# Performance work log

Measured on AMD Instinct MI355X. Metric: run time of the kernel, lower is better.

Reference implementation:

```python
import jax, jax.numpy as jnp
import numpy as np

NEG_SLOPE = 0.2


def gat_conv(x, src, dst, W, att_src, att_dst, bias, heads, out_ch, concat):
    # PyG GATConv (add_self_loops handled by caller). x: [N, in], W: [heads*out, in]
    N = x.shape[0]
    xw = (x @ W.T).reshape(N, heads, out_ch)                  # [N, H, C]
    a_src = jnp.sum(xw * att_src, axis=-1)                    # [N, H]
    a_dst = jnp.sum(xw * att_dst, axis=-1)                    # [N, H]
    alpha = a_src[src] + a_dst[dst]                           # [E, H]
    alpha = jax.nn.leaky_relu(alpha, NEG_SLOPE)
    # segment softmax over incoming edges of each dst node
    amax = jax.ops.segment_max(alpha, dst, num_segments=N)    # [N, H]
    amax = jnp.where(jnp.isfinite(amax), amax, 0.0)
    e = jnp.exp(alpha - amax[dst])                            # [E, H]
    denom = jax.ops.segment_sum(e, dst, num_segments=N)       # [N, H]
    coef = e / (denom[dst] + 1e-16)                           # [E, H]
    msg = xw[src] * coef[..., None]                           # [E, H, C]
    out = jax.ops.segment_sum(msg, dst, num_segments=N)       # [N, H, C]
    if concat:
        out = out.reshape(N, heads * out_ch)
    else:
        out = out.mean(axis=1)
    return out + bias


def setup_inputs() -> dict:
    key = jax.random.key(0)
    ks = jax.random.split(key, 10)
    N, E, F_IN, H, C = 50000, 1600000, 128, 4, 32
    x = jax.random.normal(ks[0], (N, F_IN), dtype=jnp.float32)
    edge_index = jax.random.randint(ks[1], (2, E), 0, N, dtype=jnp.int64)
    s1 = 1.0 / np.sqrt(F_IN)
    W1 = jax.random.uniform(ks[2], (H * C, F_IN), jnp.float32, -s1, s1)
    att_src1 = jax.random.normal(ks[3], (1, H, C), jnp.float32) * 0.1
    att_dst1 = jax.random.normal(ks[4], (1, H, C), jnp.float32) * 0.1
    b1 = jnp.zeros((H * C,), jnp.float32)
    s2 = 1.0 / np.sqrt(H * C)
    W2 = jax.random.uniform(ks[5], (1, H * C), jnp.float32, -s2, s2)
    att_src2 = jax.random.normal(ks[6], (1, 1, 1), jnp.float32) * 0.1
    att_dst2 = jax.random.normal(ks[7], (1, 1, 1), jnp.float32) * 0.1
    b2 = jnp.zeros((1,), jnp.float32)
    return {"x": x, "edge_index": edge_index, "W1": W1, "att_src1": att_src1,
            "att_dst1": att_dst1, "b1": b1, "W2": W2, "att_src2": att_src2,
            "att_dst2": att_dst2, "b2": b2}


def reference(x, edge_index, W1, att_src1, att_dst1, b1, W2, att_src2, att_dst2, b2):
    N = x.shape[0]
    loops = jnp.arange(N, dtype=edge_index.dtype)
    src = jnp.concatenate([edge_index[0], loops])
    dst = jnp.concatenate([edge_index[1], loops])
    h = gat_conv(x, src, dst, W1, att_src1, att_dst1, b1, heads=4, out_ch=32, concat=True)
    h = jax.nn.relu(h)
    out = gat_conv(h, src, dst, W2, att_src2, att_dst2, b2, heads=1, out_ch=1, concat=False)
    return out.squeeze(-1)
```

## Files before the change

kernel.cpp:

```cpp
#include <hip/hip_runtime.h>
#include <hip/hip_bf16.h>
#include <hip/hip_fp16.h>
#include <cstdint>
#include <cstddef>
#include <math.h>

#define NEG_SLOPE 0.2f
#define SLOTS 96
#define BSHIFT 7
#define BCAP 5632
#define SCB 768
#define ECHUNK 2176

typedef __attribute__((ext_vector_type(8))) _Float16 f16x8;
typedef __attribute__((ext_vector_type(4))) float f32x4;

__device__ __forceinline__ float lrelu(float x) { return x > 0.f ? x : NEG_SLOPE * x; }


__global__ __launch_bounds__(256) void k_init(const float* __restrict__ W1,
                                              __half* __restrict__ W1h,
                                              int* __restrict__ bin_cnt, int nbin)
{
    int i = blockIdx.x * 256 + threadIdx.x;
    if (i < 128 * 128) W1h[i] = (__half)W1[i];
    if (i < nbin) bin_cnt[i] = 0;
}

__global__ __launch_bounds__(256) void k_gemm_scatter(
    const float* __restrict__ x, const __half* __restrict__ W1h,
    const float* __restrict__ att_src, const float* __restrict__ att_dst,
    const int* __restrict__ ei, int E, int N, int GB,
    __half* __restrict__ xw, float* __restrict__ a_src, float* __restrict__ a_dst,
    int* __restrict__ bin_cnt, unsigned* __restrict__ binned)
{
    __shared__ __half tile[64][136];
    __shared__ float s_as[128], s_ad[128];

    if (blockIdx.x >= GB) {
        const int Et = E + N;
        const int nbin = (N + 127) >> BSHIFT;
        unsigned* ledge = (unsigned*)tile;
        int* lhist = (int*)(ledge + ECHUNK);
        int* lbase = lhist + nbin;
        int* lpos  = lbase + nbin;
        const int bi = blockIdx.x - GB;
        const int chunk = (Et + SCB - 1) / SCB;
        const int e0 = bi * chunk;
        const int e1 = (e0 + chunk) < Et ? (e0 + chunk) : Et;
        for (int i = threadIdx.x; i < nbin; i += 256) { lhist[i] = 0; lpos[i] = 0; }
        __syncthreads();
        for (int e = e0 + threadIdx.x; e < e1; e += 256) {
            int s, d;
            if (e < E) { s = ei[e]; d = ei[(size_t)E + e]; }
            else       { s = d = e - E; }
            unsigned b = (unsigned)d >> BSHIFT;
            ledge[e - e0] = (b << 23) | ((unsigned)(d & 127) << 16) | (unsigned)s;
            atomicAdd(&lhist[b], 1);
        }
        __syncthreads();
        for (int i = threadIdx.x; i < nbin; i += 256)
            lbase[i] = lhist[i] ? atomicAdd(&bin_cnt[i], lhist[i]) : 0;
        __syncthreads();
        const int ne = e1 - e0;
        for (int i = threadIdx.x; i < ne; i += 256) {
            unsigned w = ledge[i];
            unsigned b = w >> 23;
            int p = lbase[b] + atomicAdd(&lpos[b], 1);
            if (p < BCAP)
                binned[(size_t)b * BCAP + p] = w & 0x7FFFFFu;
        }
        return;
    }

    const int tid = threadIdx.x;
    if (tid < 128) { s_as[tid] = att_src[tid]; s_ad[tid] = att_dst[tid]; }

    const int wv = tid >> 6, lane = tid & 63;
    const int rl = lane & 15, g = lane >> 4;
    const int bm = blockIdx.x * 64;
    const int row = bm + wv * 16 + rl;
    const int rr = row < N ? row : N - 1;
    const float* xr = x + (size_t)rr * 128 + g * 8;

    f32x4 acc[8];
    #pragma unroll
    for (int i = 0; i < 8; i++) acc[i] = (f32x4){0.f, 0.f, 0.f, 0.f};

    #pragma unroll
    for (int k0 = 0; k0 < 128; k0 += 32) {
        float4 fa0 = *(const float4*)(xr + k0);
        float4 fa1 = *(const float4*)(xr + k0 + 4);
        f16x8 a;
        a[0] = (_Float16)fa0.x; a[1] = (_Float16)fa0.y;
        a[2] = (_Float16)fa0.z; a[3] = (_Float16)fa0.w;
        a[4] = (_Float16)fa1.x; a[5] = (_Float16)fa1.y;
        a[6] = (_Float16)fa1.z; a[7] = (_Float16)fa1.w;
        #pragma unroll
        for (int ct = 0; ct < 8; ct++) {
            f16x8 b = *(const f16x8*)(W1h + (size_t)(ct * 16 + rl) * 128 + k0 + g * 8);
            acc[ct] = __builtin_amdgcn_mfma_f32_16x16x32_f16(a, b, acc[ct], 0, 0, 0);
        }
    }
    #pragma unroll
    for (int ct = 0; ct < 8; ct++)
        #pragma unroll
        for (int r = 0; r < 4; r++)
            tile[wv * 16 + g * 4 + r][ct * 16 + rl] = (__half)acc[ct][r];
    __syncthreads();

    {
        int r = tid >> 2, h = tid & 3;
        int n = bm + r;
        if (n < N) {
            float4 vv[4];
            vv[0] = *(const float4*)&tile[r][h * 32];
            vv[1] = *(const float4*)&tile[r][h * 32 + 8];
            vv[2] = *(const float4*)&tile[r][h * 32 + 16];
            vv[3] = *(const float4*)&tile[r][h * 32 + 24];
            __half* xo = xw + (size_t)n * 128 + h * 32;
            *(float4*)(xo)      = vv[0];
            *(float4*)(xo + 8)  = vv[1];
            *(float4*)(xo + 16) = vv[2];
            *(float4*)(xo + 24) = vv[3];
            const float4* asp = (const float4*)(s_as + h * 32);
            const float4* adp = (const float4*)(s_ad + h * 32);
            float sv = 0.f, dv = 0.f;
            #pragma unroll
            for (int q = 0; q < 4; q++) {
                const __half2* hp = (const __half2*)&vv[q];
                float2 f0 = __half22float2(hp[0]);
                float2 f1 = __half22float2(hp[1]);
                float2 f2 = __half22float2(hp[2]);
                float2 f3 = __half22float2(hp[3]);
                float4 A0 = asp[2 * q], A1 = asp[2 * q + 1];
                float4 D0 = adp[2 * q], D1 = adp[2 * q + 1];
                sv += f0.x * A0.x + f0.y * A0.y + f1.x * A0.z + f1.y * A0.w
                    + f2.x * A1.x + f2.y * A1.y + f3.x * A1.z + f3.y * A1.w;
                dv += f0.x * D0.x + f0.y * D0.y + f1.x * D0.z + f1.y * D0.w
                    + f2.x * D1.x + f2.y * D1.y + f3.x * D1.z + f3.y * D1.w;
            }
            a_src[n * 4 + h] = sv;
            a_dst[n * 4 + h] = dv;
        }
    }
}

__global__ __launch_bounds__(256) void k_bin2bucket(
    const unsigned* __restrict__ binned, const int* __restrict__ bin_cnt,
    int* __restrict__ cnt, unsigned short* __restrict__ bucket, int N)
{
    __shared__ int lcnt[128];
    __shared__ unsigned short lb[128][SLOTS];
    const int b = blockIdx.x;
    const int base_d = b << BSHIFT;
    for (int i = threadIdx.x; i < 128; i += 256) lcnt[i] = 0;
    __syncthreads();
    int bc = bin_cnt[b]; bc = bc < BCAP ? bc : BCAP;
    const unsigned* src = binned + (size_t)b * BCAP;
    for (int t = threadIdx.x; t < bc; t += 256) {
        unsigned w = src[t];
        int dl = (int)(w >> 16);
        int p = atomicAdd(&lcnt[dl], 1);
        if (p < SLOTS) lb[dl][p] = (unsigned short)(w & 0xFFFFu);
    }
    __syncthreads();
    for (int dl = threadIdx.x; dl < 128; dl += 256) {
        int d = base_d + dl;
        if (d >= N) continue;
        int deg = lcnt[dl]; deg = deg < SLOTS ? deg : SLOTS;
        cnt[d] = deg;
        unsigned* go = (unsigned*)(bucket + (size_t)d * SLOTS);
        const unsigned* lrow = (const unsigned*)lb[dl];
        int nw = (deg + 1) >> 1;
        for (int i = 0; i < nw; i++) go[i] = lrow[i];
    }
}

__global__ __launch_bounds__(256) void k_agg(const __half* __restrict__ xw,
                                             const float* __restrict__ a_src,
                                             const float* __restrict__ a_dst,
                                             const int* __restrict__ cnt,
                                             const unsigned short* __restrict__ bucket,
                                             const float* __restrict__ b1,
                                             const float* __restrict__ W2,
                                             float* __restrict__ xw2, int N)
{
    const int wv = threadIdx.x >> 6, lane = threadIdx.x & 63;
    const int es = lane >> 4, cl = lane & 15;
    const int d = blockIdx.x * 4 + wv;
    if (d >= N) return;
    const int head = cl >> 2;
    int deg = cnt[d]; deg = deg < SLOTS ? deg : SLOTS;
    const unsigned short* brow = bucket + (size_t)d * SLOTS;

    float4 ad4 = ((const float4*)a_dst)[d];
    float adh = (head & 2) ? ((head & 1) ? ad4.w : ad4.z)
                           : ((head & 1) ? ad4.y : ad4.x);

    float acc[8] = {};
    float csum = 0.f;
    const int jb = 4 * es;
    for (int k = 0; k < deg; k += 16) {
        ushort4 ss = *(const ushort4*)(brow + k + jb);
        bool v0 = (k + jb + 0) < deg, v1 = (k + jb + 1) < deg;
        bool v2 = (k + jb + 2) < deg, v3 = (k + jb + 3) < deg;
        int s0 = v0 ? (int)ss.x : 0;
        int s1 = v1 ? (int)ss.y : 0;
        int s2 = v2 ? (int)ss.z : 0;
        int s3 = v3 ? (int)ss.w : 0;
        float ash0 = a_src[4 * s0 + head];
        float ash1 = a_src[4 * s1 + head];
        float ash2 = a_src[4 * s2 + head];
        float ash3 = a_src[4 * s3 + head];
        float4 x0 = *(const float4*)(xw + (size_t)s0 * 128 + cl * 8);
        float4 x1 = *(const float4*)(xw + (size_t)s1 * 128 + cl * 8);
        float4 x2 = *(const float4*)(xw + (size_t)s2 * 128 + cl * 8);
        float4 x3 = *(const float4*)(xw + (size_t)s3 * 128 + cl * 8);
        float c0 = v0 ? __expf(lrelu(ash0 + adh)) : 0.f;
        float c1 = v1 ? __expf(lrelu(ash1 + adh)) : 0.f;
        float c2 = v2 ? __expf(lrelu(ash2 + adh)) : 0.f;
        float c3 = v3 ? __expf(lrelu(ash3 + adh)) : 0.f;
        const __half2* h0 = (const __half2*)&x0;
        const __half2* h1 = (const __half2*)&x1;
        const __half2* h2 = (const __half2*)&x2;
        const __half2* h3 = (const __half2*)&x3;
        #pragma unroll
        for (int q = 0; q < 4; q++) {
            float2 f0 = __half22float2(h0[q]);
            float2 f1 = __half22float2(h1[q]);
            float2 f2 = __half22float2(h2[q]);
            float2 f3 = __half22float2(h3[q]);
            acc[2*q]   = fmaf(c0, f0.x, acc[2*q]);
            acc[2*q+1] = fmaf(c0, f0.y, acc[2*q+1]);
            acc[2*q]   = fmaf(c1, f1.x, acc[2*q]);
            acc[2*q+1] = fmaf(c1, f1.y, acc[2*q+1]);
            acc[2*q]   = fmaf(c2, f2.x, acc[2*q]);
            acc[2*q+1] = fmaf(c2, f2.y, acc[2*q+1]);
            acc[2*q]   = fmaf(c3, f3.x, acc[2*q]);
            acc[2*q+1] = fmaf(c3, f3.y, acc[2*q+1]);
        }
        csum += (c0 + c1) + (c2 + c3);
    }
    #pragma unroll
    for (int q = 0; q < 8; q++) {
        acc[q] += __shfl_xor(acc[q], 16);
        acc[q] += __shfl_xor(acc[q], 32);
    }
    csum += __shfl_xor(csum, 16);
    csum += __shfl_xor(csum, 32);

    float inv = 1.f / (csum + 1e-16f);
    float4 bb0 = ((const float4*)b1)[cl * 2], bb1 = ((const float4*)b1)[cl * 2 + 1];
    float4 ww0 = ((const float4*)W2)[cl * 2], ww1 = ((const float4*)W2)[cl * 2 + 1];
    float t = fmaxf(fmaf(acc[0], inv, bb0.x), 0.f) * ww0.x
            + fmaxf(fmaf(acc[1], inv, bb0.y), 0.f) * ww0.y
            + fmaxf(fmaf(acc[2], inv, bb0.z), 0.f) * ww0.z
            + fmaxf(fmaf(acc[3], inv, bb0.w), 0.f) * ww0.w
            + fmaxf(fmaf(acc[4], inv, bb1.x), 0.f) * ww1.x
            + fmaxf(fmaf(acc[5], inv, bb1.y), 0.f) * ww1.y
            + fmaxf(fmaf(acc[6], inv, bb1.z), 0.f) * ww1.z
            + fmaxf(fmaf(acc[7], inv, bb1.w), 0.f) * ww1.w;
    #pragma unroll
    for (int off = 1; off < 16; off <<= 1) t += __shfl_xor(t, off);
    if (lane == 0) xw2[d] = t;
}

__global__ __launch_bounds__(256) void k_layer2(const float* __restrict__ xw2,
                                                const int* __restrict__ cnt,
                                                const unsigned short* __restrict__ bucket,
                                                const float* __restrict__ att_src2,
                                                const float* __restrict__ att_dst2,
                                                const float* __restrict__ b2,
                                                float* __restrict__ out, int N)
{
    int grpi = (blockIdx.x * blockDim.x + threadIdx.x) >> 6;
    int lane = threadIdx.x & 63;
    int sub  = lane >> 4, li = lane & 15;
    int d    = grpi * 4 + sub;
    if (d >= N) return;
    float as2  = att_src2[0];
    float adst = xw2[d] * att_dst2[0];
    int deg = cnt[d]; deg = deg < SLOTS ? deg : SLOTS;
    const unsigned short* brow = bucket + (size_t)d * SLOTS;
    float l = 0.f, acc = 0.f;
    for (int j = 2 * li; j < deg; j += 32) {
        ushort2 ss = *(const ushort2*)(brow + j);
        int s0 = (int)ss.x;
        bool v1 = (j + 1) < deg;
        int s1 = v1 ? (int)ss.y : 0;
        float xs0 = xw2[s0];
        float xs1 = xw2[s1];
        float p0 = __expf(lrelu(fmaf(xs0, as2, adst)));
        float p1 = v1 ? __expf(lrelu(fmaf(xs1, as2, adst))) : 0.f;
        l += p0 + p1;
        acc = fmaf(p0, xs0, fmaf(p1, xs1, acc));
    }
    #pragma unroll
    for (int off = 1; off < 16; off <<= 1) {
        l   += __shfl_xor(l, off);
        acc += __shfl_xor(acc, off);
    }
    if (li == 0) out[d] = acc / (l + 1e-16f) + b2[0];
}

extern "C" void kernel_launch(void* const* d_in, const int* in_sizes, int n_in,
                              void* d_out, int out_size, void* d_ws, size_t ws_size,
                              hipStream_t stream)
{
    const float* x        = (const float*)d_in[0];
    const int*   ei       = (const int*)d_in[1];
    const float* W1       = (const float*)d_in[2];
    const float* att_src1 = (const float*)d_in[3];
    const float* att_dst1 = (const float*)d_in[4];
    const float* b1       = (const float*)d_in[5];
    const float* W2       = (const float*)d_in[6];
    const float* att_src2 = (const float*)d_in[7];
    const float* att_dst2 = (const float*)d_in[8];
    const float* b2       = (const float*)d_in[9];
    float* out = (float*)d_out;

    const int N  = in_sizes[0] / 128;
    const int E  = in_sizes[1] / 2;
    const int NBIN = (N + 127) >> BSHIFT;

    char* p = (char*)d_ws;
    auto alloc = [&](size_t bytes) {
        char* r = p;
        p += (bytes + 255) & ~(size_t)255;
        return (void*)r;
    };
    __half* xw    = (__half*)alloc((size_t)N * 128 * 2);
    __half* W1h   = (__half*)alloc((size_t)128 * 128 * 2);
    float* a_src  = (float*)alloc((size_t)N * 4 * 4);
    float* a_dst  = (float*)alloc((size_t)N * 4 * 4);
    float* xw2    = (float*)alloc((size_t)N * 4);
    int*   cnt    = (int*)alloc((size_t)N * 4);
    unsigned short* bucket = (unsigned short*)alloc((size_t)N * SLOTS * 2);
    unsigned* binned = (unsigned*)alloc((size_t)NBIN * BCAP * 4);
    int* bin_cnt  = (int*)alloc((size_t)NBIN * 4);

    const int GB = (N + 63) / 64;
    k_init        <<<64,          256, 0, stream>>>(W1, W1h, bin_cnt, NBIN);
    k_gemm_scatter<<<GB + SCB,    256, 0, stream>>>(x, W1h, att_src1, att_dst1, ei,
                                                    E, N, GB, xw, a_src, a_dst,
                                                    bin_cnt, binned);
    k_bin2bucket  <<<NBIN,        256, 0, stream>>>(binned, bin_cnt, cnt, bucket, N);
    k_agg         <<<(N + 3)/4,   256, 0, stream>>>(xw, a_src, a_dst, cnt, bucket,
                                                    b1, W2, xw2, N);
    k_layer2      <<<(N + 15)/16, 256, 0, stream>>>(xw2, cnt, bucket, att_src2,
                                                    att_dst2, b2, out, N);
}
```

Measured before the change: 193.5 us.

## Fuse bin-to-bucket conversion into layer-1 aggregation kernel using LDS buckets

Merges k_bin2bucket and k_agg into one 1024-thread kernel per 128-node bin. Each block builds its per-destination neighbor lists in shared memory, writes them out for layer 2, and then runs the layer-1 softmax aggregation straight from LDS instead of re-reading the bucket from global memory. This removes one launch and the global bucket/cnt round trip. In exchange the grid shrinks to NBIN blocks of 16 waves each, with 8 serial destinations per wave, so occupancy and load balance across CUs may suffer.

```diff
diff --git a/kernel.cpp b/kernel.cpp
--- a/kernel.cpp
+++ b/kernel.cpp
@@ -146,124 +146,127 @@
     }
 }
 
-__global__ __launch_bounds__(256) void k_bin2bucket(
+__global__ __launch_bounds__(1024) void k_aggb(
+    const __half* __restrict__ xw, const float* __restrict__ a_src,
+    const float* __restrict__ a_dst,
     const unsigned* __restrict__ binned, const int* __restrict__ bin_cnt,
-    int* __restrict__ cnt, unsigned short* __restrict__ bucket, int N)
+    int* __restrict__ cnt, unsigned short* __restrict__ bucket,
+    const float* __restrict__ b1, const float* __restrict__ W2,
+    float* __restrict__ xw2, int N)
 {
     __shared__ int lcnt[128];
     __shared__ unsigned short lb[128][SLOTS];
+    const int tid = threadIdx.x;
     const int b = blockIdx.x;
     const int base_d = b << BSHIFT;
-    for (int i = threadIdx.x; i < 128; i += 256) lcnt[i] = 0;
+
+    if (tid < 128) lcnt[tid] = 0;
     __syncthreads();
     int bc = bin_cnt[b]; bc = bc < BCAP ? bc : BCAP;
     const unsigned* src = binned + (size_t)b * BCAP;
-    for (int t = threadIdx.x; t < bc; t += 256) {
+    for (int t = tid; t < bc; t += 1024) {
         unsigned w = src[t];
         int dl = (int)(w >> 16);
         int p = atomicAdd(&lcnt[dl], 1);
         if (p < SLOTS) lb[dl][p] = (unsigned short)(w & 0xFFFFu);
     }
     __syncthreads();
-    for (int dl = threadIdx.x; dl < 128; dl += 256) {
+
+    {
+        int dl = tid >> 3, j = tid & 7;
         int d = base_d + dl;
-        if (d >= N) continue;
-        int deg = lcnt[dl]; deg = deg < SLOTS ? deg : SLOTS;
-        cnt[d] = deg;
-        unsigned* go = (unsigned*)(bucket + (size_t)d * SLOTS);
-        const unsigned* lrow = (const unsigned*)lb[dl];
-        int nw = (deg + 1) >> 1;
-        for (int i = 0; i < nw; i++) go[i] = lrow[i];
-    }
-}
-
-__global__ __launch_bounds__(256) void k_agg(const __half* __restrict__ xw,
-                                             const float* __restrict__ a_src,
-                                             const float* __restrict__ a_dst,
-                                             const int* __restrict__ cnt,
-                                             const unsigned short* __restrict__ bucket,
-                                             const float* __restrict__ b1,
-                                             const float* __restrict__ W2,
-                                             float* __restrict__ xw2, int N)
-{
-    const int wv = threadIdx.x >> 6, lane = threadIdx.x & 63;
+        if (dl < 128 && d < N) {
+            int deg = lcnt[dl]; deg = deg < SLOTS ? deg : SLOTS;
+            if (j == 0) cnt[d] = deg;
+            unsigned* go = (unsigned*)(bucket + (size_t)d * SLOTS);
+            const unsigned* lrow = (const unsigned*)lb[dl];
+            int nw = (deg + 1) >> 1;
+            for (int i = j; i < nw; i += 8) go[i] = lrow[i];
+        }
+    }
+
+    const int wv = tid >> 6, lane = tid & 63;
     const int es = lane >> 4, cl = lane & 15;
-    const int d = blockIdx.x * 4 + wv;
-    if (d >= N) return;
     const int head = cl >> 2;
-    int deg = cnt[d]; deg = deg < SLOTS ? deg : SLOTS;
-    const unsigned short* brow = bucket + (size_t)d * SLOTS;
-
-    float4 ad4 = ((const float4*)a_dst)[d];
-    float adh = (head & 2) ? ((head & 1) ? ad4.w : ad4.z)
-                           : ((head & 1) ? ad4.y : ad4.x);
-
-    float acc[8] = {};
-    float csum = 0.f;
     const int jb = 4 * es;
-    for (int k = 0; k < deg; k += 16) {
-        ushort4 ss = *(const ushort4*)(brow + k + jb);
-        bool v0 = (k + jb + 0) < deg, v1 = (k + jb + 1) < deg;
-        bool v2 = (k + jb + 2) < deg, v3 = (k + jb + 3) < deg;
-        int s0 = v0 ? (int)ss.x : 0;
-        int s1 = v1 ? (int)ss.y : 0;
-        int s2 = v2 ? (int)ss.z : 0;
-        int s3 = v3 ? (int)ss.w : 0;
-        float ash0 = a_src[4 * s0 + head];
-        float ash1 = a_src[4 * s1 + head];
-        float ash2 = a_src[4 * s2 + head];
-        float ash3 = a_src[4 * s3 + head];
-        float4 x0 = *(const float4*)(xw + (size_t)s0 * 128 + cl * 8);
-        float4 x1 = *(const float4*)(xw + (size_t)s1 * 128 + cl * 8);
-        float4 x2 = *(const float4*)(xw + (size_t)s2 * 128 + cl * 8);
-        float4 x3 = *(const float4*)(xw + (size_t)s3 * 128 + cl * 8);
-        float c0 = v0 ? __expf(lrelu(ash0 + adh)) : 0.f;
-        float c1 = v1 ? __expf(lrelu(ash1 + adh)) : 0.f;
-        float c2 = v2 ? __expf(lrelu(ash2 + adh)) : 0.f;
-        float c3 = v3 ? __expf(lrelu(ash3 + adh)) : 0.f;
-        const __half2* h0 = (const __half2*)&x0;
-        const __half2* h1 = (const __half2*)&x1;
-        const __half2* h2 = (const __half2*)&x2;
-        const __half2* h3 = (const __half2*)&x3;
-        #pragma unroll
-        for (int q = 0; q < 4; q++) {
-            float2 f0 = __half22float2(h0[q]);
-            float2 f1 = __half22float2(h1[q]);
-            float2 f2 = __half22float2(h2[q]);
-            float2 f3 = __half22float2(h3[q]);
-            acc[2*q]   = fmaf(c0, f0.x, acc[2*q]);
-            acc[2*q+1] = fmaf(c0, f0.y, acc[2*q+1]);
-            acc[2*q]   = fmaf(c1, f1.x, acc[2*q]);
-            acc[2*q+1] = fmaf(c1, f1.y, acc[2*q+1]);
-            acc[2*q]   = fmaf(c2, f2.x, acc[2*q]);
-            acc[2*q+1] = fmaf(c2, f2.y, acc[2*q+1]);
-            acc[2*q]   = fmaf(c3, f3.x, acc[2*q]);
-            acc[2*q+1] = fmaf(c3, f3.y, acc[2*q+1]);
-        }
-        csum += (c0 + c1) + (c2 + c3);
-    }
-    #pragma unroll
-    for (int q = 0; q < 8; q++) {
-        acc[q] += __shfl_xor(acc[q], 16);
-        acc[q] += __shfl_xor(acc[q], 32);
-    }
-    csum += __shfl_xor(csum, 16);
-    csum += __shfl_xor(csum, 32);
-
-    float inv = 1.f / (csum + 1e-16f);
+
     float4 bb0 = ((const float4*)b1)[cl * 2], bb1 = ((const float4*)b1)[cl * 2 + 1];
     float4 ww0 = ((const float4*)W2)[cl * 2], ww1 = ((const float4*)W2)[cl * 2 + 1];
-    float t = fmaxf(fmaf(acc[0], inv, bb0.x), 0.f) * ww0.x
-            + fmaxf(fmaf(acc[1], inv, bb0.y), 0.f) * ww0.y
-            + fmaxf(fmaf(acc[2], inv, bb0.z), 0.f) * ww0.z
-            + fmaxf(fmaf(acc[3], inv, bb0.w), 0.f) * ww0.w
-            + fmaxf(fmaf(acc[4], inv, bb1.x), 0.f) * ww1.x
-            + fmaxf(fmaf(acc[5], inv, bb1.y), 0.f) * ww1.y
-            + fmaxf(fmaf(acc[6], inv, bb1.z), 0.f) * ww1.z
-            + fmaxf(fmaf(acc[7], inv, bb1.w), 0.f) * ww1.w;
-    #pragma unroll
-    for (int off = 1; off < 16; off <<= 1) t += __shfl_xor(t, off);
-    if (lane == 0) xw2[d] = t;
+
+    for (int i = 0; i < 8; i++) {
+        int dl = wv * 8 + i;
+        int d = base_d + dl;
+        if (d >= N) break;
+        int deg = lcnt[dl]; deg = deg < SLOTS ? deg : SLOTS;
+        const unsigned short* brow = lb[dl];
+
+        float4 ad4 = ((const float4*)a_dst)[d];
+        float adh = (head & 2) ? ((head & 1) ? ad4.w : ad4.z)
+                               : ((head & 1) ? ad4.y : ad4.x);
+        float acc[8] = {};
+        float csum = 0.f;
+        for (int k = 0; k < deg; k += 16) {
+            ushort4 ss = *(const ushort4*)(brow + k + jb);
+            bool v0 = (k + jb + 0) < deg, v1 = (k + jb + 1) < deg;
+            bool v2 = (k + jb + 2) < deg, v3 = (k + jb + 3) < deg;
+            int s0 = v0 ? (int)ss.x : 0;
+            int s1 = v1 ? (int)ss.y : 0;
+            int s2 = v2 ? (int)ss.z : 0;
+            int s3 = v3 ? (int)ss.w : 0;
+            float ash0 = a_src[4 * s0 + head];
+            float ash1 = a_src[4 * s1 + head];
+            float ash2 = a_src[4 * s2 + head];
+            float ash3 = a_src[4 * s3 + head];
+            float4 x0 = *(const float4*)(xw + (size_t)s0 * 128 + cl * 8);
+            float4 x1 = *(const float4*)(xw + (size_t)s1 * 128 + cl * 8);
+            float4 x2 = *(const float4*)(xw + (size_t)s2 * 128 + cl * 8);
+            float4 x3 = *(const float4*)(xw + (size_t)s3 * 128 + cl * 8);
+            float c0 = v0 ? __expf(lrelu(ash0 + adh)) : 0.f;
+            float c1 = v1 ? __expf(lrelu(ash1 + adh)) : 0.f;
+            float c2 = v2 ? __expf(lrelu(ash2 + adh)) : 0.f;
+            float c3 = v3 ? __expf(lrelu(ash3 + adh)) : 0.f;
+            const __half2* h0 = (const __half2*)&x0;
+            const __half2* h1 = (const __half2*)&x1;
+            const __half2* h2 = (const __half2*)&x2;
+            const __half2* h3 = (const __half2*)&x3;
+            #pragma unroll
+            for (int q = 0; q < 4; q++) {
+                float2 f0 = __half22float2(h0[q]);
+                float2 f1 = __half22float2(h1[q]);
+                float2 f2 = __half22float2(h2[q]);
+                float2 f3 = __half22float2(h3[q]);
+                acc[2*q]   = fmaf(c0, f0.x, acc[2*q]);
+                acc[2*q+1] = fmaf(c0, f0.y, acc[2*q+1]);
+                acc[2*q]   = fmaf(c1, f1.x, acc[2*q]);
+                acc[2*q+1] = fmaf(c1, f1.y, acc[2*q+1]);
+                acc[2*q]   = fmaf(c2, f2.x, acc[2*q]);
+                acc[2*q+1] = fmaf(c2, f2.y, acc[2*q+1]);
+                acc[2*q]   = fmaf(c3, f3.x, acc[2*q]);
+                acc[2*q+1] = fmaf(c3, f3.y, acc[2*q+1]);
+            }
+            csum += (c0 + c1) + (c2 + c3);
+        }
+        #pragma unroll
+        for (int q = 0; q < 8; q++) {
+            acc[q] += __shfl_xor(acc[q], 16);
+            acc[q] += __shfl_xor(acc[q], 32);
+        }
+        csum += __shfl_xor(csum, 16);
+        csum += __shfl_xor(csum, 32);
+
+        float inv = 1.f / (csum + 1e-16f);
+        float t = fmaxf(fmaf(acc[0], inv, bb0.x), 0.f) * ww0.x
+                + fmaxf(fmaf(acc[1], inv, bb0.y), 0.f) * ww0.y
+                + fmaxf(fmaf(acc[2], inv, bb0.z), 0.f) * ww0.z
+                + fmaxf(fmaf(acc[3], inv, bb0.w), 0.f) * ww0.w
+                + fmaxf(fmaf(acc[4], inv, bb1.x), 0.f) * ww1.x
+                + fmaxf(fmaf(acc[5], inv, bb1.y), 0.f) * ww1.y
+                + fmaxf(fmaf(acc[6], inv, bb1.z), 0.f) * ww1.z
+                + fmaxf(fmaf(acc[7], inv, bb1.w), 0.f) * ww1.w;
+        #pragma unroll
+        for (int off = 1; off < 16; off <<= 1) t += __shfl_xor(t, off);
+        if (lane == 0) xw2[d] = t;
+    }
 }
 
 __global__ __launch_bounds__(256) void k_layer2(const float* __restrict__ xw2,
@@ -341,13 +344,13 @@
     int* bin_cnt  = (int*)alloc((size_t)NBIN * 4);
 
     const int GB = (N + 63) / 64;
-    k_init        <<<64,          256, 0, stream>>>(W1, W1h, bin_cnt, NBIN);
-    k_gemm_scatter<<<GB + SCB,    256, 0, stream>>>(x, W1h, att_src1, att_dst1, ei,
-                                                    E, N, GB, xw, a_src, a_dst,
-                                                    bin_cnt, binned);
-    k_bin2bucket  <<<NBIN,        256, 0, stream>>>(binned, bin_cnt, cnt, bucket, N);
-    k_agg         <<<(N + 3)/4,   256, 0, stream>>>(xw, a_src, a_dst, cnt, bucket,
-                                                    b1, W2, xw2, N);
-    k_layer2      <<<(N + 15)/16, 256, 0, stream>>>(xw2, cnt, bucket, att_src2,
-                                                    att_dst2, b2, out, N);
-}
+    k_init        <<<64,          256,  0, stream>>>(W1, W1h, bin_cnt, NBIN);
+    k_gemm_scatter<<<GB + SCB,    256,  0, stream>>>(x, W1h, att_src1, att_dst1, ei,
+                                                     E, N, GB, xw, a_src, a_dst,
+                                                     bin_cnt, binned);
+    k_aggb        <<<NBIN,        1024, 0, stream>>>(xw, a_src, a_dst, binned,
+                                                     bin_cnt, cnt, bucket,
+                                                     b1, W2, xw2, N);
+    k_layer2      <<<(N + 15)/16, 256,  0, stream>>>(xw2, cnt, bucket, att_src2,
+                                                     att_dst2, b2, out, N);
+}
```

Result: slower. 203.4 us (+5.1%).
